# Kernel tuning notes

Hardware: AMD Instinct MI355X
Metric: run time of the kernel (lower is better)

The kernel has to match this reference:

```python
import jax, jax.numpy as jnp
import numpy as np

EMBED_DIM = 1280
NUM_HEADS = 32
HEAD_DIM = EMBED_DIM // NUM_HEADS  # 40
SCALING = HEAD_DIM ** -0.5
BSZ, TGT_LEN, PAST_LEN = 2, 1024, 1024


def setup_inputs() -> dict:
    key = jax.random.key(0)
    ks = jax.random.split(key, 8)
    w_scale = 1.0 / np.sqrt(EMBED_DIM)
    return {
        "inputs": jax.random.normal(ks[0], (BSZ, TGT_LEN, EMBED_DIM), jnp.float32),
        "past_key": jax.random.normal(ks[1], (BSZ, NUM_HEADS, PAST_LEN, HEAD_DIM), jnp.float32),
        "past_value": jax.random.normal(ks[2], (BSZ, NUM_HEADS, PAST_LEN, HEAD_DIM), jnp.float32),
        "Wq": jax.random.normal(ks[3], (EMBED_DIM, EMBED_DIM), jnp.float32) * w_scale,
        "bq": jnp.zeros((EMBED_DIM,), jnp.float32),
        "Wk": jax.random.normal(ks[4], (EMBED_DIM, EMBED_DIM), jnp.float32) * w_scale,
        "bk": jnp.zeros((EMBED_DIM,), jnp.float32),
        "Wv": jax.random.normal(ks[5], (EMBED_DIM, EMBED_DIM), jnp.float32) * w_scale,
        "bv": jnp.zeros((EMBED_DIM,), jnp.float32),
        "Wo": jax.random.normal(ks[6], (EMBED_DIM, EMBED_DIM), jnp.float32) * w_scale,
        "bo": jnp.zeros((EMBED_DIM,), jnp.float32),
    }


def _shape(x, bsz):
    # [b, s, e] -> [b, h, s, d]
    return x.reshape(bsz, -1, NUM_HEADS, HEAD_DIM).transpose(0, 2, 1, 3)


def reference(inputs, past_key, past_value, Wq, bq, Wk, bk, Wv, bv, Wo, bo):
    bsz, tgt_len, _ = inputs.shape
    # projections (dropout rate is 0 -> identity)
    q = _shape((inputs @ Wq + bq) * SCALING, bsz)        # [b,h,t,d]
    k_new = _shape(inputs @ Wk + bk, bsz)                # [b,h,t,d]
    v_new = _shape(inputs @ Wv + bv, bsz)
    # KV-cache concat along seq axis
    key_states = jnp.concatenate([past_key, k_new], axis=2)    # [b,h,s,d]
    value_states = jnp.concatenate([past_value, v_new], axis=2)
    # attention: QK^T -> softmax -> AV (full score matrix, as original)
    attn_weights = jnp.einsum('bhid,bhjd->bhij', q, key_states)  # [b,h,t,s]
    attn_probs = jax.nn.softmax(attn_weights, axis=-1)
    attn_output = jnp.einsum('bhij,bhjd->bhid', attn_probs, value_states)  # [b,h,t,d]
    attn_output = attn_output.transpose(0, 2, 1, 3).reshape(bsz, tgt_len, EMBED_DIM)
    attn_output = attn_output @ Wo + bo
    return attn_output, key_states, value_states
```

## Files before the change

### kernel.cpp

```cpp
#include <hip/hip_runtime.h>
#include <hip/hip_bf16.h>

#define ED 1280
#define NH 32
#define HD 40
#define BSZ 2
#define TL 1024
#define SEQ 2048
#define SCALING 0.15811388300841897f

typedef __bf16 bf16x8 __attribute__((ext_vector_type(8)));
typedef float floatx4 __attribute__((ext_vector_type(4)));
typedef unsigned short ushort;

__device__ __forceinline__ ushort f2bf(float f) {
    __hip_bfloat16 h = __float2bfloat16(f);
    return *(ushort*)&h;
}
__device__ __forceinline__ unsigned pk2(float a, float b) {
    return (unsigned)f2bf(a) | ((unsigned)f2bf(b) << 16);
}

#define ASYNC16(g, l)                                                                 \
    __builtin_amdgcn_global_load_lds((const __attribute__((address_space(1))) void*)(g), \
                                     (__attribute__((address_space(3))) void*)(l), 16, 0, 0)

__global__ void convert_x_zero(const float* X, ushort* Xb, ushort* Qb) {
    int bid = blockIdx.x;
    if (bid < 2560) {
        int i = (bid * 256 + threadIdx.x) * 4;
        float4 v = *(const float4*)&X[i];
        ushort4 o;
        o.x = f2bf(v.x); o.y = f2bf(v.y); o.z = f2bf(v.z); o.w = f2bf(v.w);
        *(ushort4*)&Xb[i] = o;
    } else {
        int i = ((bid - 2560) * 256 + threadIdx.x) * 8;
        uint4 z = {0, 0, 0, 0};
        *(uint4*)&Qb[i] = z;
    }
}

__global__ void transpose_w(const float* w0, const float* w1,
                            const float* w2, const float* w3, ushort* wt) {
    __shared__ float tile[32][33];
    int z = blockIdx.z;
    const float* w = (z == 0) ? w0 : (z == 1) ? w1 : (z == 2) ? w2 : w3;
    ushort* o = wt + (size_t)z * ED * ED;
    int n0 = blockIdx.x * 32, k0 = blockIdx.y * 32;
    int tx = threadIdx.x, ty = threadIdx.y;
#pragma unroll
    for (int i = ty; i < 32; i += 8) tile[i][tx] = w[(k0 + i) * ED + n0 + tx];
    __syncthreads();
#pragma unroll
    for (int i = ty; i < 32; i += 8) o[(n0 + i) * ED + k0 + tx] = f2bf(tile[tx][i]);
}

__global__ void copy_past(const float* PK, const float* PV, float* keyOut, float* valOut) {
    int idx = blockIdx.x * 256 + threadIdx.x;
    int which = idx >= 655360;
    int f4 = which ? idx - 655360 : idx;
    const float4* src = (const float4*)(which ? PV : PK);
    float4* dst = (float4*)(which ? valOut : keyOut);
    int bhj = f4 / 10, c4 = f4 - bhj * 10;
    int bh = bhj >> 10, j = bhj & 1023;
    dst[(bh * SEQ + j) * 10 + c4] = src[f4];
}

__global__ void prep_k(const float* keyOut, ushort* Kb16) {
    int idx = blockIdx.x * 256 + threadIdx.x;
    int row = idx / 6, j = idx - row * 6;
    uint4 o = {0, 0, 0, 0};
    if (j < 5) {
        const float* s = &keyOut[(size_t)row * 40 + j * 8];
        float4 a = *(const float4*)s;
        float4 b = *(const float4*)(s + 4);
        o.x = pk2(a.x, a.y); o.y = pk2(a.z, a.w);
        o.z = pk2(b.x, b.y); o.w = pk2(b.z, b.w);
    }
    *(uint4*)&Kb16[(size_t)row * 48 + j * 8] = o;
}

__global__ void prep_v(const float* valOut, ushort* Vt16) {
    __shared__ ushort T[48 * 72];
    int bh = blockIdx.x, st = blockIdx.y;
    int tid = threadIdx.x;
    for (int i = tid; i < 8 * 72; i += 256) {
        int dr = i / 72, k = i - dr * 72;
        T[(40 + dr) * 72 + k] = (dr == 0) ? 0x3F80 : 0;
    }
    const float* src = valOut + ((size_t)bh * SEQ + st * 64) * 40;
    for (int i = tid; i < 640; i += 256) {
        int key = i / 10, c = i - key * 10;
        float4 v = *(const float4*)&src[key * 40 + c * 4];
        T[(c * 4 + 0) * 72 + key] = f2bf(v.x);
        T[(c * 4 + 1) * 72 + key] = f2bf(v.y);
        T[(c * 4 + 2) * 72 + key] = f2bf(v.z);
        T[(c * 4 + 3) * 72 + key] = f2bf(v.w);
    }
    __syncthreads();
    ushort* dst = Vt16 + (size_t)bh * 48 * 2048 + st * 64;
    for (int i = tid; i < 384; i += 256) {
        int d = i >> 3, c = i & 7;
        *(uint4*)&dst[(size_t)d * 2048 + c * 8] = *(const uint4*)&T[d * 72 + c * 8];
    }
}

__device__ __forceinline__ void gemm_core(const ushort* A, const ushort* Bt,
                                          ushort* As, ushort* Bs,
                                          int m0, int n0, floatx4 acc[4][4]) {
    int tidx = threadIdx.x;
    int wave = tidx >> 6, lane = tidx & 63;
    int wm = (wave >> 1) * 64, wn = (wave & 1) * 64;
    int fr = lane & 15, kq = lane >> 4;
    for (int k0 = 0; k0 < ED; k0 += 32) {
#pragma unroll
        for (int p = 0; p < 2; ++p) {
            int flat = p * 2048 + tidx * 8;
            int r = flat >> 5, c = flat & 31;
            ASYNC16(&A[(m0 + r) * ED + k0 + c], &As[flat]);
            ASYNC16(&Bt[(n0 + r) * ED + k0 + c], &Bs[flat]);
        }
        __syncthreads();
        bf16x8 a[4], b[4];
#pragma unroll
        for (int mi = 0; mi < 4; ++mi) a[mi] = *(const bf16x8*)&As[(wm + mi * 16 + fr) * 32 + kq * 8];
#pragma unroll
        for (int ni = 0; ni < 4; ++ni) b[ni] = *(const bf16x8*)&Bs[(wn + ni * 16 + fr) * 32 + kq * 8];
#pragma unroll
        for (int mi = 0; mi < 4; ++mi)
#pragma unroll
            for (int ni = 0; ni < 4; ++ni)
                acc[mi][ni] = __builtin_amdgcn_mfma_f32_16x16x32_bf16(a[mi], b[ni], acc[mi][ni], 0, 0, 0);
        __syncthreads();
    }
}

__global__ __launch_bounds__(256) void gemm_qkv(const ushort* Xb, const ushort* Wt,
                                                const float* bq, const float* bk,
                                                const float* bv, ushort* Qb,
                                                float* keyOut, float* valOut) {
    __shared__ ushort As[128 * 32], Bs[128 * 32];
    int z = blockIdx.z;
    const ushort* Bt = Wt + (size_t)z * ED * ED;
    const float* bias = (z == 0) ? bq : (z == 1) ? bk : bv;
    int m0 = blockIdx.y * 128, n0 = blockIdx.x * 128;
    floatx4 acc[4][4] = {};
    gemm_core(Xb, Bt, As, Bs, m0, n0, acc);
    int lane = threadIdx.x & 63, wave = threadIdx.x >> 6;
    int wm = (wave >> 1) * 64, wn = (wave & 1) * 64;
    int cq = lane >> 4, cc = lane & 15;
#pragma unroll
    for (int mi = 0; mi < 4; ++mi)
#pragma unroll
        for (int ni = 0; ni < 4; ++ni) {
            int col = n0 + wn + ni * 16 + cc;
            float bvf = bias[col];
            int h = col / HD, dh = col - h * HD;
#pragma unroll
            for (int r = 0; r < 4; ++r) {
                int row = m0 + wm + mi * 16 + cq * 4 + r;
                int b = row >> 10, t = row & 1023;
                float v = acc[mi][ni][r] + bvf;
                if (z == 0) {
                    Qb[(((b * NH + h) * TL) + t) * 64 + dh] = f2bf(v * SCALING);
                } else {
                    int idx = ((b * NH + h) * SEQ + TL + t) * HD + dh;
                    (z == 1 ? keyOut : valOut)[idx] = v;
                }
            }
        }
}

__global__ __launch_bounds__(256) void gemm_out(const ushort* A, const ushort* Bt,
                                                const float* bias, float* out) {
    __shared__ ushort As[128 * 32], Bs[128 * 32];
    int m0 = blockIdx.y * 128, n0 = blockIdx.x * 128;
    floatx4 acc[4][4] = {};
    gemm_core(A, Bt, As, Bs, m0, n0, acc);
    int lane = threadIdx.x & 63, wave = threadIdx.x >> 6;
    int wm = (wave >> 1) * 64, wn = (wave & 1) * 64;
    int cq = lane >> 4, cc = lane & 15;
#pragma unroll
    for (int mi = 0; mi < 4; ++mi)
#pragma unroll
        for (int ni = 0; ni < 4; ++ni) {
            int col = n0 + wn + ni * 16 + cc;
            float bvf = bias[col];
#pragma unroll
            for (int r = 0; r < 4; ++r) {
                int row = m0 + wm + mi * 16 + cq * 4 + r;
                out[row * ED + col] = acc[mi][ni][r] + bvf;
            }
        }
}

__global__ __launch_bounds__(256) void attn_mfma(const ushort* Qb, const ushort* Kb16,
                                                 const ushort* Vt16, ushort* O) {
    __shared__ ushort Ks[64 * 72];
    __shared__ ushort Vs[48 * 72];
    __shared__ ushort Ps[4 * 16 * 72];

    int bh = blockIdx.x, b = bh >> 5, h = bh & 31;
    int tid = threadIdx.x, wave = tid >> 6, lane = tid & 63;
    int col = lane & 15, quad = lane >> 4;
    int qbase = blockIdx.y * 64 + wave * 16;

    for (int i = tid; i < 64 * 24; i += 256) {
        int r = i / 24, c = i - r * 24;
        Ks[r * 72 + 48 + c] = 0;
    }

    bf16x8 qa[2];
#pragma unroll
    for (int ks = 0; ks < 2; ++ks)
        qa[ks] = *(const bf16x8*)(Qb + ((size_t)bh * TL + qbase + col) * 64 + ks * 32 + quad * 8);

    const uint4* Ksrc = (const uint4*)(Kb16 + (size_t)bh * SEQ * 48);
    const uint4* Vsrc = (const uint4*)(Vt16 + (size_t)bh * 48 * SEQ);

    floatx4 Oacc[3] = {};
    ushort* pw = Ps + wave * (16 * 72);

    for (int t = 0; t < SEQ / 64; ++t) {
        __syncthreads();
        for (int i = tid; i < 384; i += 256) {
            int key = i / 6, c = i - key * 6;
            *(uint4*)&Ks[key * 72 + c * 8] = Ksrc[t * 384 + i];
            int d = i >> 3, c2 = i & 7;
            *(uint4*)&Vs[d * 72 + c2 * 8] = Vsrc[d * 256 + t * 8 + c2];
        }
        __syncthreads();

        floatx4 S[4] = {};
#pragma unroll
        for (int ks = 0; ks < 2; ++ks) {
            bf16x8 kb[4];
#pragma unroll
            for (int n = 0; n < 4; ++n)
                kb[n] = *(const bf16x8*)&Ks[(n * 16 + col) * 72 + ks * 32 + quad * 8];
#pragma unroll
            for (int n = 0; n < 4; ++n)
                S[n] = __builtin_amdgcn_mfma_f32_16x16x32_bf16(qa[ks], kb[n], S[n], 0, 0, 0);
        }

#pragma unroll
        for (int n = 0; n < 4; ++n)
#pragma unroll
            for (int r = 0; r < 4; ++r) {
                float p = exp2f(fmaf(S[n][r], 1.442695041f, -17.31234049f));
                pw[(quad * 4 + r) * 72 + n * 16 + col] = f2bf(p);
            }

#pragma unroll
        for (int ks = 0; ks < 2; ++ks) {
            bf16x8 pa = *(const bf16x8*)&pw[col * 72 + ks * 32 + quad * 8];
#pragma unroll
            for (int n = 0; n < 3; ++n) {
                bf16x8 vb = *(const bf16x8*)&Vs[(n * 16 + col) * 72 + ks * 32 + quad * 8];
                Oacc[n] = __builtin_amdgcn_mfma_f32_16x16x32_bf16(pa, vb, Oacc[n], 0, 0, 0);
            }
        }
    }

    float linv[4];
#pragma unroll
    for (int r = 0; r < 4; ++r)
        linv[r] = 1.f / __shfl(Oacc[2][r], (lane & 48) + 8, 64);
#pragma unroll
    for (int n = 0; n < 3; ++n) {
        int d = n * 16 + col;
        if (d < HD) {
#pragma unroll
            for (int r = 0; r < 4; ++r) {
                int q = qbase + quad * 4 + r;
                O[(size_t)(b * TL + q) * ED + h * HD + d] = f2bf(Oacc[n][r] * linv[r]);
            }
        }
    }
}

extern "C" void kernel_launch(void* const* d_in, const int* in_sizes, int n_in,
                              void* d_out, int out_size, void* d_ws, size_t ws_size,
                              hipStream_t stream) {
    const float* X  = (const float*)d_in[0];
    const float* PK = (const float*)d_in[1];
    const float* PV = (const float*)d_in[2];
    const float* Wq = (const float*)d_in[3];
    const float* bq = (const float*)d_in[4];
    const float* Wk = (const float*)d_in[5];
    const float* bk = (const float*)d_in[6];
    const float* Wv = (const float*)d_in[7];
    const float* bv = (const float*)d_in[8];
    const float* Wo = (const float*)d_in[9];
    const float* bo = (const float*)d_in[10];

    float* out = (float*)d_out;
    float* keyOut = out + 2621440;
    float* valOut = keyOut + 5242880;

    ushort* ws   = (ushort*)d_ws;
    ushort* Wt   = ws;
    ushort* Qb   = Wt + 4 * (ED * ED);
    ushort* Kb16 = Qb + (size_t)65536 * 64;
    ushort* Vt16 = Kb16 + (size_t)131072 * 48;
    ushort* Xb   = Vt16 + (size_t)64 * 48 * 2048;
    ushort* Aws  = Xb;

    convert_x_zero<<<dim3(4608), dim3(256), 0, stream>>>(X, Xb, Qb);
    transpose_w<<<dim3(40, 40, 4), dim3(32, 8), 0, stream>>>(Wq, Wk, Wv, Wo, Wt);
    copy_past<<<dim3(5120), dim3(256), 0, stream>>>(PK, PV, keyOut, valOut);
    gemm_qkv<<<dim3(10, 16, 3), dim3(256), 0, stream>>>(Xb, Wt, bq, bk, bv, Qb, keyOut, valOut);
    prep_k<<<dim3(3072), dim3(256), 0, stream>>>(keyOut, Kb16);
    prep_v<<<dim3(64, 32), dim3(256), 0, stream>>>(valOut, Vt16);
    attn_mfma<<<dim3(64, 16), dim3(256), 0, stream>>>(Qb, Kb16, Vt16, Aws);
    gemm_out<<<dim3(10, 16), dim3(256), 0, stream>>>(Aws, Wt + 3 * (ED * ED), bo, out);
}
```

Baseline: 285.0 us.

## Keep softmax probabilities in registers, double KV tile, prefetch next tile

Computes the score tile as K·Qᵀ so each lane's probabilities already sit in the MFMA A-operand layout. They are packed into registers directly, which removes the per-wave P staging through shared memory. It also doubles the key tile to 128 with a permuted K row layout, and prefetches the next tile's K/V into registers while the current tile computes. It sets launch bounds for 4 blocks per CU. The costs are higher register pressure and a more intricate row-permutation mapping, which must match the MFMA output layout exactly.

```diff
diff --git a/kernel.cpp b/kernel.cpp
--- a/kernel.cpp
+++ b/kernel.cpp
@@ -12,6 +12,7 @@
 typedef __bf16 bf16x8 __attribute__((ext_vector_type(8)));
 typedef float floatx4 __attribute__((ext_vector_type(4)));
 typedef unsigned short ushort;
+typedef ushort ushortx8 __attribute__((ext_vector_type(8)));
 
 __device__ __forceinline__ ushort f2bf(float f) {
     __hip_bfloat16 h = __float2bfloat16(f);
@@ -194,20 +195,19 @@
         }
 }
 
-__global__ __launch_bounds__(256) void attn_mfma(const ushort* Qb, const ushort* Kb16,
-                                                 const ushort* Vt16, ushort* O) {
-    __shared__ ushort Ks[64 * 72];
-    __shared__ ushort Vs[48 * 72];
-    __shared__ ushort Ps[4 * 16 * 72];
+__global__ __launch_bounds__(256, 4) void attn_mfma(const ushort* Qb, const ushort* Kb16,
+                                                    const ushort* Vt16, ushort* O) {
+    __shared__ ushort Ks[128 * 72];
+    __shared__ ushort Vs[48 * 136];
 
     int bh = blockIdx.x, b = bh >> 5, h = bh & 31;
     int tid = threadIdx.x, wave = tid >> 6, lane = tid & 63;
     int col = lane & 15, quad = lane >> 4;
     int qbase = blockIdx.y * 64 + wave * 16;
 
-    for (int i = tid; i < 64 * 24; i += 256) {
-        int r = i / 24, c = i - r * 24;
-        Ks[r * 72 + 48 + c] = 0;
+    {
+        uint4 z = {0, 0, 0, 0};
+        *(uint4*)&Ks[(tid >> 1) * 72 + 48 + (tid & 1) * 8] = z;
     }
 
     bf16x8 qa[2];
@@ -218,46 +218,68 @@
     const uint4* Ksrc = (const uint4*)(Kb16 + (size_t)bh * SEQ * 48);
     const uint4* Vsrc = (const uint4*)(Vt16 + (size_t)bh * 48 * SEQ);
 
+    int kof[3], klin[3], vof[3], vlin[3];
+#pragma unroll
+    for (int u = 0; u < 3; ++u) {
+        int i = u * 256 + tid;
+        int key = i / 6, c = i - key * 6;
+        int srow = 32 * (key >> 5) + 16 * ((key >> 2) & 1) + 4 * ((key >> 3) & 3) + (key & 3);
+        kof[u] = srow * 72 + c * 8;
+        klin[u] = i;
+        int d = u * 16 + (tid >> 4), c2 = tid & 15;
+        vof[u] = d * 136 + c2 * 8;
+        vlin[u] = d * 256 + c2;
+    }
+
+    uint4 kr[3], vr[3];
+#pragma unroll
+    for (int u = 0; u < 3; ++u) kr[u] = Ksrc[klin[u]];
+#pragma unroll
+    for (int u = 0; u < 3; ++u) vr[u] = Vsrc[vlin[u]];
+
     floatx4 Oacc[3] = {};
-    ushort* pw = Ps + wave * (16 * 72);
-
-    for (int t = 0; t < SEQ / 64; ++t) {
+
+#pragma unroll 1
+    for (int t = 0; t < SEQ / 128; ++t) {
         __syncthreads();
-        for (int i = tid; i < 384; i += 256) {
-            int key = i / 6, c = i - key * 6;
-            *(uint4*)&Ks[key * 72 + c * 8] = Ksrc[t * 384 + i];
-            int d = i >> 3, c2 = i & 7;
-            *(uint4*)&Vs[d * 72 + c2 * 8] = Vsrc[d * 256 + t * 8 + c2];
+#pragma unroll
+        for (int u = 0; u < 3; ++u) *(uint4*)&Ks[kof[u]] = kr[u];
+#pragma unroll
+        for (int u = 0; u < 3; ++u) *(uint4*)&Vs[vof[u]] = vr[u];
+        if (t < SEQ / 128 - 1) {
+#pragma unroll
+            for (int u = 0; u < 3; ++u) kr[u] = Ksrc[(t + 1) * 768 + klin[u]];
+#pragma unroll
+            for (int u = 0; u < 3; ++u) vr[u] = Vsrc[(t + 1) * 16 + vlin[u]];
         }
         __syncthreads();
 
-        floatx4 S[4] = {};
-#pragma unroll
-        for (int ks = 0; ks < 2; ++ks) {
-            bf16x8 kb[4];
-#pragma unroll
-            for (int n = 0; n < 4; ++n)
-                kb[n] = *(const bf16x8*)&Ks[(n * 16 + col) * 72 + ks * 32 + quad * 8];
-#pragma unroll
-            for (int n = 0; n < 4; ++n)
-                S[n] = __builtin_amdgcn_mfma_f32_16x16x32_bf16(qa[ks], kb[n], S[n], 0, 0, 0);
-        }
-
-#pragma unroll
-        for (int n = 0; n < 4; ++n)
-#pragma unroll
-            for (int r = 0; r < 4; ++r) {
-                float p = exp2f(fmaf(S[n][r], 1.442695041f, -17.31234049f));
-                pw[(quad * 4 + r) * 72 + n * 16 + col] = f2bf(p);
-            }
-
-#pragma unroll
-        for (int ks = 0; ks < 2; ++ks) {
-            bf16x8 pa = *(const bf16x8*)&pw[col * 72 + ks * 32 + quad * 8];
-#pragma unroll
-            for (int n = 0; n < 3; ++n) {
-                bf16x8 vb = *(const bf16x8*)&Vs[(n * 16 + col) * 72 + ks * 32 + quad * 8];
-                Oacc[n] = __builtin_amdgcn_mfma_f32_16x16x32_bf16(pa, vb, Oacc[n], 0, 0, 0);
+        floatx4 S[8] = {};
+#pragma unroll
+        for (int ks = 0; ks < 2; ++ks)
+#pragma unroll
+            for (int n = 0; n < 8; ++n) {
+                bf16x8 kb = *(const bf16x8*)&Ks[(n * 16 + col) * 72 + ks * 32 + quad * 8];
+                S[n] = __builtin_amdgcn_mfma_f32_16x16x32_bf16(kb, qa[ks], S[n], 0, 0, 0);
+            }
+
+#pragma unroll
+        for (int ks = 0; ks < 4; ++ks) {
+            ushortx8 pp;
+#pragma unroll
+            for (int half = 0; half < 2; ++half) {
+                int n = 2 * ks + half;
+#pragma unroll
+                for (int r = 0; r < 4; ++r) {
+                    float p = exp2f(fmaf(S[n][r], 1.442695041f, -17.31234049f));
+                    pp[half * 4 + r] = f2bf(p);
+                }
+            }
+            bf16x8 pa = __builtin_bit_cast(bf16x8, pp);
+#pragma unroll
+            for (int no = 0; no < 3; ++no) {
+                bf16x8 vb = *(const bf16x8*)&Vs[(no * 16 + col) * 136 + ks * 32 + quad * 8];
+                Oacc[no] = __builtin_amdgcn_mfma_f32_16x16x32_bf16(pa, vb, Oacc[no], 0, 0, 0);
             }
         }
     }
```

Result: slower. 336.7 us (+18.2%).
